# Kernel tuning notes

Measured on AMD Instinct MI355X. Metric: run time of the kernel, lower is better.

Reference implementation:

```python
import jax, jax.numpy as jnp
import numpy as np

NEG = -1e30  # finite stand-in for -inf so softmax grads stay clean


def setup_inputs() -> dict:
    key = jax.random.key(0)
    k1, k2 = jax.random.split(key)
    C, D = 8192, 512
    gt_class_embeddings = jax.random.normal(k1, (C, D), dtype=jnp.float32)
    w = jax.random.normal(k2, (C, D), dtype=jnp.float32)
    return {"gt_class_embeddings": gt_class_embeddings, "w": w}


def reference(gt_class_embeddings, w):
    # L2-normalize class embeddings, cosine-similarity matrix S (diag == 1)
    G = gt_class_embeddings / jnp.linalg.norm(gt_class_embeddings, axis=-1, keepdims=True)
    S = G @ G.T  # [C, C]
    C = S.shape[0]
    off_diag = ~jnp.eye(C, dtype=bool)

    # seSoftmax: per-row softmax over entries != 1 (off-diagonal); diagonal stays 1
    P = jax.nn.softmax(jnp.where(off_diag, S, NEG), axis=-1)
    S2 = jnp.where(off_diag, P, 1.0)

    # argsort(-S2)[1] == most similar (diag value 1 always ranks first),
    # argsort(-S2)[-1] == least similar == row min (softmax values < 1)
    ms = jnp.argmax(jnp.where(off_diag, S2, NEG), axis=-1)  # [C]
    ls = jnp.argmin(jnp.where(off_diag, S2, -NEG), axis=-1)  # [C]

    rows = jnp.arange(C)
    margin = S2[rows, ms] - S2[rows, ls]  # [C]

    d_ms = jnp.sqrt(jnp.sum((w - w[ms]) ** 2, axis=-1))  # [C]
    d_ls = jnp.sqrt(jnp.sum((w - w[ls]) ** 2, axis=-1))  # [C]

    loss = jnp.mean(jnp.maximum(0.0, d_ms - d_ls + margin))
    return loss
```

## Files before the change

### kernel.cpp

```cpp
#include <hip/hip_runtime.h>
#include <math.h>

#define CDIM 8192
#define DDIM 512
#define NEGF -3.0e38f
#define POSF  3.0e38f

#define BM 128
#define NSLOT (CDIM / BM)

typedef __attribute__((ext_vector_type(8))) short bf16x8;
typedef __attribute__((ext_vector_type(4))) float f32x4;

__device__ __forceinline__ unsigned short f2bf(float x) {
    unsigned int u = __float_as_uint(x);
    u += 0x7fffu + ((u >> 16) & 1u);
    return (unsigned short)(u >> 16);
}
__device__ __forceinline__ float bf2f(unsigned short h) {
    return __uint_as_float(((unsigned int)h) << 16);
}
__device__ __forceinline__ void gld16(const void* g, void* l) {
    __builtin_amdgcn_global_load_lds(
        (__attribute__((address_space(1))) void*)(void*)g,
        (__attribute__((address_space(3))) void*)l, 16, 0, 0);
}

__global__ __launch_bounds__(256) void k_prep(const float* __restrict__ g,
                                              unsigned short* __restrict__ hi,
                                              unsigned short* __restrict__ lo) {
    const int wave = threadIdx.x >> 6;
    const int lane = threadIdx.x & 63;
    const int row = blockIdx.x * 4 + wave;
    const float4* src = (const float4*)(g + (size_t)row * DDIM);
    const float4 a = src[lane * 2];
    const float4 b = src[lane * 2 + 1];
    float s = a.x * a.x + a.y * a.y + a.z * a.z + a.w * a.w +
              b.x * b.x + b.y * b.y + b.z * b.z + b.w * b.w;
#pragma unroll
    for (int m = 1; m < 64; m <<= 1) s += __shfl_xor(s, m, 64);
    const float rn = rsqrtf(s);
    const float y[8] = {a.x * rn, a.y * rn, a.z * rn, a.w * rn,
                        b.x * rn, b.y * rn, b.z * rn, b.w * rn};
    unsigned int hv[4], lv[4];
#pragma unroll
    for (int i = 0; i < 4; ++i) {
        const unsigned short h0 = f2bf(y[2 * i]);
        const unsigned short h1 = f2bf(y[2 * i + 1]);
        const unsigned short l0 = f2bf(y[2 * i] - bf2f(h0));
        const unsigned short l1 = f2bf(y[2 * i + 1] - bf2f(h1));
        hv[i] = (unsigned int)h0 | ((unsigned int)h1 << 16);
        lv[i] = (unsigned int)l0 | ((unsigned int)l1 << 16);
    }
    uint4* dh = (uint4*)(hi + (size_t)row * DDIM + lane * 8);
    uint4* dl = (uint4*)(lo + (size_t)row * DDIM + lane * 8);
    *dh = make_uint4(hv[0], hv[1], hv[2], hv[3]);
    *dl = make_uint4(lv[0], lv[1], lv[2], lv[3]);
}

__device__ __constant__ unsigned char OSUP[28] = {
    1, 2, 10,   3, 11, 19,   4, 12, 20,   28, 5, 13,
    21, 29, 37, 6,   14, 22, 30, 38,   46, 7, 15, 23,   31, 39, 47, 55};

__global__ __launch_bounds__(256, 3) void k_simstats(
    const unsigned short* __restrict__ ghi, const unsigned short* __restrict__ glo,
    float* __restrict__ pmax, float* __restrict__ pmin, float* __restrict__ pZ,
    int* __restrict__ pamax, int* __restrict__ pamin) {
    const int bid = blockIdx.x;
    const int xcd = bid & 7;
    const int off = bid >> 3;
    int I, J;
    if (xcd < 4) {
        if (off < 72) {
            const int s = xcd * 2 + (off >= 36);
            const int u = (off >= 36) ? off - 36 : off;
            int jj = 0;
            while ((jj + 1) * (jj + 2) / 2 <= u) ++jj;
            const int ii = u - jj * (jj + 1) / 2;
            I = s * 8 + ii; J = s * 8 + jj;
        } else {
            const int sup = (off - 72) >> 6;
            const int u = (off - 72) & 63;
            const int code = OSUP[xcd * 3 + sup];
            I = (code >> 3) * 8 + (u & 7);
            J = (code & 7) * 8 + (u >> 3);
        }
    } else {
        if (off >= 256) return;
        const int sup = off >> 6;
        const int u = off & 63;
        const int code = OSUP[12 + (xcd - 4) * 4 + sup];
        I = (code >> 3) * 8 + (u & 7);
        J = (code & 7) * 8 + (u >> 3);
    }

    __shared__ unsigned short SH[6 * 4096];
    const int t = threadIdx.x;
    const int wave = t >> 6;
    const int lane = t & 63;
    const int lanelo = lane & 15;
    const int quad = lane >> 4;
    const int wr = wave & 1;
    const int wc = wave >> 1;

    const int srow = t >> 2;
    const int scolb = ((t & 3) ^ ((t >> 3) & 3)) << 4;

    const int fsl = (quad ^ ((lanelo >> 1) & 3)) << 3;
    const int aoff = (wr * 64 + lanelo) * 32 + fsl;
    const int boff = (wc * 64 + lanelo) * 32 + fsl;

    float* rm  = (float*)SH;
    float* rz  = rm + 256;
    float* rmn = rz + 256;
    int*   ra  = (int*)(rmn + 256);
    int*   ran = ra + 256;
    float* cm  = (float*)(SH + 4096);
    float* cz  = cm + 256;
    float* cmn = cz + 256;
    int*   ca  = (int*)(cmn + 256);
    int*   can = ca + 256;

    const int i0 = I * BM;
    const int j0 = J * BM;
    const bool isdiag = (I == J);

    f32x4 acc[4][4];
#pragma unroll
    for (int rt = 0; rt < 4; ++rt)
#pragma unroll
        for (int ct = 0; ct < 4; ++ct)
            acc[rt][ct] = (f32x4){0.f, 0.f, 0.f, 0.f};

    const char* baseAh = (const char*)ghi + (size_t)(i0 + srow) * 1024 + scolb;
    const char* baseAl = (const char*)glo + (size_t)(i0 + srow) * 1024 + scolb;
    const char* baseBh = (const char*)ghi + (size_t)(j0 + srow) * 1024 + scolb;
    const char* baseBl = (const char*)glo + (size_t)(j0 + srow) * 1024 + scolb;

    auto STG = [&](const char* gbase, int ks, int s) {
        char* const d = (char*)SH + s * 8192 + t * 16;
        const size_t cb = (size_t)ks * 64;
        gld16(gbase + cb, d);
        gld16(gbase + 65536 + cb, d + 4096);
    };

    const int rAH[6] = {0, 4, 2, 1, 5, 3};
    const int rBL[6] = {1, 5, 3, 0, 4, 2};
    const int rBH[6] = {2, 1, 5, 3, 0, 4};
    const int rAL[6] = {3, 0, 4, 2, 1, 5};

    STG(baseAh, 0, 0);
    STG(baseBl, 0, 1);
    STG(baseBh, 0, 2);
    STG(baseAl, 0, 3);

    bf16x8 ah[4], bh[4];
#pragma unroll
    for (int ks = 0; ks < 16; ++ks) {
        const int m = ks % 6;
        const int m2 = (ks + 1) % 6;
        if (ks < 15) { STG(baseAh, ks + 1, rAH[m2]); STG(baseBl, ks + 1, rBL[m2]); }
        if (ks < 15) asm volatile("s_waitcnt vmcnt(8)" ::: "memory");
        else         asm volatile("s_waitcnt vmcnt(4)" ::: "memory");
        __builtin_amdgcn_s_barrier();
        asm volatile("" ::: "memory");
        {
            const unsigned short* pA = SH + rAH[m] * 4096;
            const unsigned short* pB = SH + rBL[m] * 4096;
            bf16x8 bl[4];
#pragma unroll
            for (int rt = 0; rt < 4; ++rt) ah[rt] = *(const bf16x8*)&pA[aoff + rt * 512];
#pragma unroll
            for (int ct = 0; ct < 4; ++ct) bl[ct] = *(const bf16x8*)&pB[boff + ct * 512];
            __builtin_amdgcn_s_setprio(1);
#pragma unroll
            for (int ct = 0; ct < 4; ++ct)
#pragma unroll
                for (int rt = 0; rt < 4; ++rt)
                    acc[rt][ct] = __builtin_amdgcn_mfma_f32_16x16x32_bf16(
                        ah[rt], bl[ct], acc[rt][ct], 0, 0, 0);
            __builtin_amdgcn_s_setprio(0);
        }
        asm volatile("s_waitcnt lgkmcnt(0)" ::: "memory");
        __builtin_amdgcn_s_barrier();
        asm volatile("" ::: "memory");
        if (ks < 15) STG(baseBh, ks + 1, rBH[m2]);
        if (ks < 15) asm volatile("s_waitcnt vmcnt(8)" ::: "memory");
        else         asm volatile("s_waitcnt vmcnt(2)" ::: "memory");
        __builtin_amdgcn_s_barrier();
        asm volatile("" ::: "memory");
        {
            const unsigned short* pB = SH + rBH[m] * 4096;
#pragma unroll
            for (int ct = 0; ct < 4; ++ct) bh[ct] = *(const bf16x8*)&pB[boff + ct * 512];
            __builtin_amdgcn_s_setprio(1);
#pragma unroll
            for (int ct = 0; ct < 4; ++ct)
#pragma unroll
                for (int rt = 0; rt < 4; ++rt)
                    acc[rt][ct] = __builtin_amdgcn_mfma_f32_16x16x32_bf16(
                        ah[rt], bh[ct], acc[rt][ct], 0, 0, 0);
            __builtin_amdgcn_s_setprio(0);
        }
        asm volatile("s_waitcnt lgkmcnt(0)" ::: "memory");
        __builtin_amdgcn_s_barrier();
        asm volatile("" ::: "memory");
        if (ks < 15) STG(baseAl, ks + 1, rAL[m2]);
        if (ks < 15) asm volatile("s_waitcnt vmcnt(8)" ::: "memory");
        else         asm volatile("s_waitcnt vmcnt(0)" ::: "memory");
        __builtin_amdgcn_s_barrier();
        asm volatile("" ::: "memory");
        {
            const unsigned short* pA = SH + rAL[m] * 4096;
            bf16x8 al[4];
#pragma unroll
            for (int rt = 0; rt < 4; ++rt) al[rt] = *(const bf16x8*)&pA[aoff + rt * 512];
            __builtin_amdgcn_s_setprio(1);
#pragma unroll
            for (int ct = 0; ct < 4; ++ct)
#pragma unroll
                for (int rt = 0; rt < 4; ++rt)
                    acc[rt][ct] = __builtin_amdgcn_mfma_f32_16x16x32_bf16(
                        al[rt], bh[ct], acc[rt][ct], 0, 0, 0);
            __builtin_amdgcn_s_setprio(0);
        }
        asm volatile("s_waitcnt lgkmcnt(0)" ::: "memory");
        __builtin_amdgcn_s_barrier();
        asm volatile("" ::: "memory");
    }

#pragma unroll
    for (int rt = 0; rt < 4; ++rt) {
#pragma unroll
        for (int r = 0; r < 4; ++r) {
            const int lrow = wr * 64 + rt * 16 + quad * 4 + r;
            float tmax = NEGF; int targ = 0;
            float tmin = POSF; int targn = 0;
            if (isdiag) {
                const int gi = i0 + lrow;
#pragma unroll
                for (int ct = 0; ct < 4; ++ct) {
                    const int gj = j0 + wc * 64 + ct * 16 + lanelo;
                    const float v = acc[rt][ct][r];
                    const bool dg = (gj == gi);
                    const float vM = dg ? NEGF : v;
                    const float vm = dg ? POSF : v;
                    if (vM > tmax) { tmax = vM; targ = gj; }
                    if (vm < tmin) { tmin = vm; targn = gj; }
                }
            } else {
#pragma unroll
                for (int ct = 0; ct < 4; ++ct) {
                    const int gj = j0 + wc * 64 + ct * 16 + lanelo;
                    const float v = acc[rt][ct][r];
                    if (v > tmax) { tmax = v; targ = gj; }
                    if (v < tmin) { tmin = v; targn = gj; }
                }
            }
#pragma unroll
            for (int msk = 1; msk < 16; msk <<= 1) {
                const float v2 = __shfl_xor(tmax, msk, 64);
                const int i2 = __shfl_xor(targ, msk, 64);
                if (v2 > tmax) { tmax = v2; targ = i2; }
                const float v3 = __shfl_xor(tmin, msk, 64);
                const int i3 = __shfl_xor(targn, msk, 64);
                if (v3 < tmin) { tmin = v3; targn = i3; }
            }
            if (lanelo == 0) {
                const int o = wc * 128 + lrow;
                rm[o] = tmax; rmn[o] = tmin;
                ra[o] = targ; ran[o] = targn;
            }
        }
    }

    if (!isdiag) {
#pragma unroll
        for (int ct = 0; ct < 4; ++ct) {
            const int lcol = wc * 64 + ct * 16 + lanelo;
            float tmax = NEGF; int targ = 0;
            float tmin = POSF; int targn = 0;
#pragma unroll
            for (int rt = 0; rt < 4; ++rt)
#pragma unroll
                for (int r = 0; r < 4; ++r) {
                    const int gi = i0 + wr * 64 + rt * 16 + quad * 4 + r;
                    const float v = acc[rt][ct][r];
                    if (v > tmax) { tmax = v; targ = gi; }
                    if (v < tmin) { tmin = v; targn = gi; }
                }
#pragma unroll
            for (int msk = 16; msk < 64; msk <<= 1) {
                const float m2v = __shfl_xor(tmax, msk, 64);
                const int i2 = __shfl_xor(targ, msk, 64);
                if (m2v > tmax) { tmax = m2v; targ = i2; }
                const float mn2 = __shfl_xor(tmin, msk, 64);
                const int in2 = __shfl_xor(targn, msk, 64);
                if (mn2 < tmin) { tmin = mn2; targn = in2; }
            }
            if (quad == 0) {
                const int o = wr * 128 + lcol;
                cm[o] = tmax; cmn[o] = tmin;
                ca[o] = targ; can[o] = targn;
            }
        }
    }

#pragma unroll
    for (int rt = 0; rt < 4; ++rt)
#pragma unroll
        for (int ct = 0; ct < 4; ++ct)
#pragma unroll
            for (int r = 0; r < 4; ++r)
                acc[rt][ct][r] = __expf(acc[rt][ct][r] - 1.f);
    if (isdiag && wr == wc) {
#pragma unroll
        for (int rt = 0; rt < 4; ++rt)
#pragma unroll
            for (int r = 0; r < 4; ++r)
                if (lanelo == quad * 4 + r) acc[rt][rt][r] = 0.f;
    }

#pragma unroll
    for (int rt = 0; rt < 4; ++rt)
#pragma unroll
        for (int r = 0; r < 4; ++r) {
            float s = acc[rt][0][r] + acc[rt][1][r] +
                      acc[rt][2][r] + acc[rt][3][r];
#pragma unroll
            for (int msk = 1; msk < 16; msk <<= 1) s += __shfl_xor(s, msk, 64);
            if (lanelo == 0)
                rz[wc * 128 + wr * 64 + rt * 16 + quad * 4 + r] = s;
        }

    if (!isdiag) {
#pragma unroll
        for (int ct = 0; ct < 4; ++ct) {
            float s = 0.f;
#pragma unroll
            for (int rt = 0; rt < 4; ++rt)
                s += acc[rt][ct][0] + acc[rt][ct][1] +
                     acc[rt][ct][2] + acc[rt][ct][3];
#pragma unroll
            for (int msk = 16; msk < 64; msk <<= 1) s += __shfl_xor(s, msk, 64);
            if (quad == 0)
                cz[wr * 128 + wc * 64 + ct * 16 + lanelo] = s;
        }
    }

    __syncthreads();

    if (t < BM) {
        const float m0 = rm[t], m1 = rm[128 + t];
        float vmax = m0; int imax = ra[t];
        if (m1 > vmax) { vmax = m1; imax = ra[128 + t]; }
        float vmin = rmn[t]; int imin = ran[t];
        if (rmn[128 + t] < vmin) { vmin = rmn[128 + t]; imin = ran[128 + t]; }
        const size_t o = (size_t)J * CDIM + i0 + t;
        pmax[o] = vmax; pmin[o] = vmin; pZ[o] = rz[t] + rz[128 + t];
        pamax[o] = imax; pamin[o] = imin;
    } else if (!isdiag) {
        const int tt = t - BM;
        const float m0 = cm[tt], m1 = cm[128 + tt];
        float vmax = m0; int imax = ca[tt];
        if (m1 > vmax) { vmax = m1; imax = ca[128 + tt]; }
        float vmin = cmn[tt]; int imin = can[tt];
        if (cmn[128 + tt] < vmin) { vmin = cmn[128 + tt]; imin = can[128 + tt]; }
        const size_t o = (size_t)I * CDIM + j0 + tt;
        pmax[o] = vmax; pmin[o] = vmin; pZ[o] = cz[tt] + cz[128 + tt];
        pamax[o] = imax; pamin[o] = imin;
    }
}

__global__ __launch_bounds__(256) void k_lossc(
    const float* __restrict__ pmax, const float* __restrict__ pmin,
    const float* __restrict__ pZ, const int* __restrict__ pamax,
    const int* __restrict__ pamin, const float* __restrict__ w,
    float* __restrict__ vals) {
    const int wave = threadIdx.x >> 6;
    const int lane = threadIdx.x & 63;
    const int row = blockIdx.x * 4 + wave;
    const size_t o = (size_t)lane * CDIM + row;
    float v = pmax[o]; int a = pamax[o];
    float u = pmin[o]; int b = pamin[o];
    float z = pZ[o];
#pragma unroll
    for (int msk = 1; msk < 64; msk <<= 1) {
        const float v2 = __shfl_xor(v, msk, 64);
        const int i2 = __shfl_xor(a, msk, 64);
        if (v2 > v) { v = v2; a = i2; }
        const float v3 = __shfl_xor(u, msk, 64);
        const int i3 = __shfl_xor(b, msk, 64);
        if (v3 < u) { u = v3; b = i3; }
        z += __shfl_xor(z, msk, 64);
    }
    const float margin = (1.f - __expf(u - v)) * __expf(v - 1.f) / z;
    const int jm = a, jl = b;

    const float4* wi = (const float4*)(w + (size_t)row * DDIM);
    const float4* wm = (const float4*)(w + (size_t)jm * DDIM);
    const float4* wl = (const float4*)(w + (size_t)jl * DDIM);
    float sm = 0.f, sl = 0.f;
#pragma unroll
    for (int h = 0; h < 2; ++h) {
        const int idx = h * 64 + lane;
        const float4 x = wi[idx];
        const float4 y = wm[idx];
        const float4 c = wl[idx];
        float d;
        d = x.x - y.x; sm = fmaf(d, d, sm);
        d = x.y - y.y; sm = fmaf(d, d, sm);
        d = x.z - y.z; sm = fmaf(d, d, sm);
        d = x.w - y.w; sm = fmaf(d, d, sm);
        d = x.x - c.x; sl = fmaf(d, d, sl);
        d = x.y - c.y; sl = fmaf(d, d, sl);
        d = x.z - c.z; sl = fmaf(d, d, sl);
        d = x.w - c.w; sl = fmaf(d, d, sl);
    }
#pragma unroll
    for (int msk = 1; msk < 64; msk <<= 1) {
        sm += __shfl_xor(sm, msk, 64);
        sl += __shfl_xor(sl, msk, 64);
    }
    if (lane == 0) {
        const float val = sqrtf(sm) - sqrtf(sl) + margin;
        vals[row] = val > 0.f ? val : 0.f;
    }
}

__global__ __launch_bounds__(256) void k_final(const float* __restrict__ vals,
                                               float* __restrict__ out) {
    __shared__ float red[256];
    float s = 0.f;
    for (int i = threadIdx.x; i < CDIM; i += 256) s += vals[i];
    red[threadIdx.x] = s;
    __syncthreads();
#pragma unroll
    for (int k = 128; k > 0; k >>= 1) {
        if (threadIdx.x < (unsigned)k) red[threadIdx.x] += red[threadIdx.x + k];
        __syncthreads();
    }
    if (threadIdx.x == 0) out[0] = red[0] * (1.0f / CDIM);
}

extern "C" void kernel_launch(void* const* d_in, const int* in_sizes, int n_in,
                              void* d_out, int out_size, void* d_ws, size_t ws_size,
                              hipStream_t stream) {
    const float* g = (const float*)d_in[0];
    const float* w = (const float*)d_in[1];
    float* out = (float*)d_out;

    unsigned short* ghi = (unsigned short*)d_ws;
    unsigned short* glo = ghi + (size_t)CDIM * DDIM;
    float* p = (float*)(glo + (size_t)CDIM * DDIM);
    float* pmax = p;      p += (size_t)NSLOT * CDIM;
    float* pmin = p;      p += (size_t)NSLOT * CDIM;
    float* pZ = p;        p += (size_t)NSLOT * CDIM;
    int* pamax = (int*)p; p += (size_t)NSLOT * CDIM;
    int* pamin = (int*)p; p += (size_t)NSLOT * CDIM;
    float* vals = p;      p += CDIM;

    k_prep<<<CDIM / 4, 256, 0, stream>>>(g, ghi, glo);
    k_simstats<<<2112, 256, 0, stream>>>(ghi, glo, pmax, pmin, pZ, pamax, pamin);
    k_lossc<<<CDIM / 4, 256, 0, stream>>>(pmax, pmin, pZ, pamax, pamin, w, vals);
    k_final<<<1, 256, 0, stream>>>(vals, out);
}
```

Before: 228.4 us.

## Use 256x128 tiles with 512-thread blocks and triple-buffered K pipeline

Enlarges the symmetric similarity tile from 128x128 to 256x128 per block with 8 waves, halving the block count and replacing the XCD-aware supertile schedule with a simple triangular enumeration over (I, J) pairs. The K loop moves from a six-slot per-operand rotation to a three-stage buffer holding the full A and B hi/lo tiles, prefetching two steps ahead. Diagonal handling is generalized to two partial-diagonal tile types. The aim is more operand reuse per loaded byte and fewer blocks, at the cost of much larger LDS use (144KB per block) and lower occupancy, and the simpler schedule drops the L2/XCD locality mapping.

```diff
diff --git a/kernel.cpp b/kernel.cpp
--- a/kernel.cpp
+++ b/kernel.cpp
@@ -6,8 +6,7 @@
 #define NEGF -3.0e38f
 #define POSF  3.0e38f
 
-#define BM 128
-#define NSLOT (CDIM / BM)
+#define NSLOT 64
 
 typedef __attribute__((ext_vector_type(8))) short bf16x8;
 typedef __attribute__((ext_vector_type(4))) float f32x4;
@@ -58,50 +57,30 @@
     *dl = make_uint4(lv[0], lv[1], lv[2], lv[3]);
 }
 
-__device__ __constant__ unsigned char OSUP[28] = {
-    1, 2, 10,   3, 11, 19,   4, 12, 20,   28, 5, 13,
-    21, 29, 37, 6,   14, 22, 30, 38,   46, 7, 15, 23,   31, 39, 47, 55};
-
-__global__ __launch_bounds__(256, 3) void k_simstats(
+__global__ __launch_bounds__(512, 2) void k_simstats(
     const unsigned short* __restrict__ ghi, const unsigned short* __restrict__ glo,
     float* __restrict__ pmax, float* __restrict__ pmin, float* __restrict__ pZ,
     int* __restrict__ pamax, int* __restrict__ pamin) {
     const int bid = blockIdx.x;
-    const int xcd = bid & 7;
-    const int off = bid >> 3;
-    int I, J;
-    if (xcd < 4) {
-        if (off < 72) {
-            const int s = xcd * 2 + (off >= 36);
-            const int u = (off >= 36) ? off - 36 : off;
-            int jj = 0;
-            while ((jj + 1) * (jj + 2) / 2 <= u) ++jj;
-            const int ii = u - jj * (jj + 1) / 2;
-            I = s * 8 + ii; J = s * 8 + jj;
-        } else {
-            const int sup = (off - 72) >> 6;
-            const int u = (off - 72) & 63;
-            const int code = OSUP[xcd * 3 + sup];
-            I = (code >> 3) * 8 + (u & 7);
-            J = (code & 7) * 8 + (u >> 3);
-        }
-    } else {
-        if (off >= 256) return;
-        const int sup = off >> 6;
-        const int u = off & 63;
-        const int code = OSUP[12 + (xcd - 4) * 4 + sup];
-        I = (code >> 3) * 8 + (u & 7);
-        J = (code & 7) * 8 + (u >> 3);
-    }
-
-    __shared__ unsigned short SH[6 * 4096];
+    const int e = (bid & 7) * 132 + (bid >> 3);
+    int J = 0, base = 0;
+    while (true) {
+        const int cnt = (J >> 1) + 1;
+        if (e < base + cnt) break;
+        base += cnt; ++J;
+    }
+    const int I = e - base;
+    const bool typeD0 = (J == 2 * I);
+    const bool typeD1 = (J == 2 * I + 1);
+
+    __shared__ unsigned short SH[3 * 24576];
     const int t = threadIdx.x;
     const int wave = t >> 6;
     const int lane = t & 63;
     const int lanelo = lane & 15;
     const int quad = lane >> 4;
-    const int wr = wave & 1;
-    const int wc = wave >> 1;
+    const int wr = wave >> 1;
+    const int wc = wave & 1;
 
     const int srow = t >> 2;
     const int scolb = ((t & 3) ^ ((t >> 3) & 3)) << 4;
@@ -111,19 +90,18 @@
     const int boff = (wc * 64 + lanelo) * 32 + fsl;
 
     float* rm  = (float*)SH;
-    float* rz  = rm + 256;
-    float* rmn = rz + 256;
-    int*   ra  = (int*)(rmn + 256);
-    int*   ran = ra + 256;
-    float* cm  = (float*)(SH + 4096);
-    float* cz  = cm + 256;
-    float* cmn = cz + 256;
-    int*   ca  = (int*)(cmn + 256);
-    int*   can = ca + 256;
-
-    const int i0 = I * BM;
-    const int j0 = J * BM;
-    const bool isdiag = (I == J);
+    float* rmn = rm + 512;
+    float* rz  = rmn + 512;
+    int*   ra  = (int*)(rz + 512);
+    int*   ran = ra + 512;
+    float* cm  = (float*)(ran + 512);
+    float* cmn = cm + 512;
+    float* cz  = cmn + 512;
+    int*   ca  = (int*)(cz + 512);
+    int*   can = ca + 512;
+
+    const int i0 = I * 256;
+    const int j0 = J * 128;
 
     f32x4 acc[4][4];
 #pragma unroll
@@ -137,41 +115,43 @@
     const char* baseBh = (const char*)ghi + (size_t)(j0 + srow) * 1024 + scolb;
     const char* baseBl = (const char*)glo + (size_t)(j0 + srow) * 1024 + scolb;
 
-    auto STG = [&](const char* gbase, int ks, int s) {
-        char* const d = (char*)SH + s * 8192 + t * 16;
+    auto STG_A = [&](int ks, int b, int half) {
+        char* d = (char*)SH + b * 49152 + half * 16384 + t * 16;
+        const char* gb = half ? baseAl : baseAh;
         const size_t cb = (size_t)ks * 64;
-        gld16(gbase + cb, d);
-        gld16(gbase + 65536 + cb, d + 4096);
+        gld16(gb + cb, d);
+        gld16(gb + 131072 + cb, d + 8192);
     };
-
-    const int rAH[6] = {0, 4, 2, 1, 5, 3};
-    const int rBL[6] = {1, 5, 3, 0, 4, 2};
-    const int rBH[6] = {2, 1, 5, 3, 0, 4};
-    const int rAL[6] = {3, 0, 4, 2, 1, 5};
-
-    STG(baseAh, 0, 0);
-    STG(baseBl, 0, 1);
-    STG(baseBh, 0, 2);
-    STG(baseAl, 0, 3);
-
-    bf16x8 ah[4], bh[4];
+    auto STG_B = [&](int ks, int b, int half) {
+        char* d = (char*)SH + b * 49152 + 32768 + half * 8192 + t * 16;
+        const char* gb = half ? baseBl : baseBh;
+        gld16(gb + (size_t)ks * 64, d);
+    };
+
+    STG_A(0, 0, 0); STG_A(0, 0, 1); STG_B(0, 0, 0); STG_B(0, 0, 1);
+    STG_A(1, 1, 0); STG_A(1, 1, 1); STG_B(1, 1, 0); STG_B(1, 1, 1);
+    asm volatile("s_waitcnt vmcnt(6)" ::: "memory");
+    __builtin_amdgcn_s_barrier();
+    asm volatile("" ::: "memory");
+
 #pragma unroll
     for (int ks = 0; ks < 16; ++ks) {
-        const int m = ks % 6;
-        const int m2 = (ks + 1) % 6;
-        if (ks < 15) { STG(baseAh, ks + 1, rAH[m2]); STG(baseBl, ks + 1, rBL[m2]); }
-        if (ks < 15) asm volatile("s_waitcnt vmcnt(8)" ::: "memory");
-        else         asm volatile("s_waitcnt vmcnt(4)" ::: "memory");
-        __builtin_amdgcn_s_barrier();
-        asm volatile("" ::: "memory");
+        const unsigned short* buf = SH + (ks % 3) * 24576;
+        const int sb = (ks + 2) % 3;
+        const bool st = (ks <= 13);
+        bf16x8 ah[4], bh[4];
         {
-            const unsigned short* pA = SH + rAH[m] * 4096;
-            const unsigned short* pB = SH + rBL[m] * 4096;
+            if (st) STG_A(ks + 2, sb, 0);
             bf16x8 bl[4];
 #pragma unroll
-            for (int rt = 0; rt < 4; ++rt) ah[rt] = *(const bf16x8*)&pA[aoff + rt * 512];
-#pragma unroll
-            for (int ct = 0; ct < 4; ++ct) bl[ct] = *(const bf16x8*)&pB[boff + ct * 512];
+            for (int rt = 0; rt < 4; ++rt)
+                ah[rt] = *(const bf16x8*)&buf[aoff + rt * 512];
+#pragma unroll
+            for (int ct = 0; ct < 4; ++ct)
+                bl[ct] = *(const bf16x8*)&buf[20480 + boff + ct * 512];
+            asm volatile("" ::: "memory");
+            __builtin_amdgcn_s_barrier();
+            asm volatile("s_waitcnt lgkmcnt(0)" ::: "memory");
             __builtin_amdgcn_s_setprio(1);
 #pragma unroll
             for (int ct = 0; ct < 4; ++ct)
@@ -180,19 +160,18 @@
                     acc[rt][ct] = __builtin_amdgcn_mfma_f32_16x16x32_bf16(
                         ah[rt], bl[ct], acc[rt][ct], 0, 0, 0);
             __builtin_amdgcn_s_setprio(0);
-        }
-        asm volatile("s_waitcnt lgkmcnt(0)" ::: "memory");
-        __builtin_amdgcn_s_barrier();
-        asm volatile("" ::: "memory");
-        if (ks < 15) STG(baseBh, ks + 1, rBH[m2]);
-        if (ks < 15) asm volatile("s_waitcnt vmcnt(8)" ::: "memory");
-        else         asm volatile("s_waitcnt vmcnt(2)" ::: "memory");
-        __builtin_amdgcn_s_barrier();
-        asm volatile("" ::: "memory");
+            asm volatile("" ::: "memory");
+            __builtin_amdgcn_s_barrier();
+            asm volatile("" ::: "memory");
+        }
         {
-            const unsigned short* pB = SH + rBH[m] * 4096;
-#pragma unroll
-            for (int ct = 0; ct < 4; ++ct) bh[ct] = *(const bf16x8*)&pB[boff + ct * 512];
+            if (st) STG_A(ks + 2, sb, 1);
+#pragma unroll
+            for (int ct = 0; ct < 4; ++ct)
+                bh[ct] = *(const bf16x8*)&buf[16384 + boff + ct * 512];
+            asm volatile("" ::: "memory");
+            __builtin_amdgcn_s_barrier();
+            asm volatile("s_waitcnt lgkmcnt(0)" ::: "memory");
             __builtin_amdgcn_s_setprio(1);
 #pragma unroll
             for (int ct = 0; ct < 4; ++ct)
@@ -201,20 +180,21 @@
                     acc[rt][ct] = __builtin_amdgcn_mfma_f32_16x16x32_bf16(
                         ah[rt], bh[ct], acc[rt][ct], 0, 0, 0);
             __builtin_amdgcn_s_setprio(0);
-        }
-        asm volatile("s_waitcnt lgkmcnt(0)" ::: "memory");
-        __builtin_amdgcn_s_barrier();
-        asm volatile("" ::: "memory");
-        if (ks < 15) STG(baseAl, ks + 1, rAL[m2]);
-        if (ks < 15) asm volatile("s_waitcnt vmcnt(8)" ::: "memory");
-        else         asm volatile("s_waitcnt vmcnt(0)" ::: "memory");
-        __builtin_amdgcn_s_barrier();
-        asm volatile("" ::: "memory");
+            asm volatile("" ::: "memory");
+            __builtin_amdgcn_s_barrier();
+            asm volatile("" ::: "memory");
+        }
         {
-            const unsigned short* pA = SH + rAL[m] * 4096;
+            if (st) { STG_B(ks + 2, sb, 0); STG_B(ks + 2, sb, 1); }
             bf16x8 al[4];
 #pragma unroll
-            for (int rt = 0; rt < 4; ++rt) al[rt] = *(const bf16x8*)&pA[aoff + rt * 512];
+            for (int rt = 0; rt < 4; ++rt)
+                al[rt] = *(const bf16x8*)&buf[8192 + aoff + rt * 512];
+            if (ks <= 13) asm volatile("s_waitcnt vmcnt(6)" ::: "memory");
+            else if (ks == 14) asm volatile("s_waitcnt vmcnt(0)" ::: "memory");
+            asm volatile("" ::: "memory");
+            __builtin_amdgcn_s_barrier();
+            asm volatile("s_waitcnt lgkmcnt(0)" ::: "memory");
             __builtin_amdgcn_s_setprio(1);
 #pragma unroll
             for (int ct = 0; ct < 4; ++ct)
@@ -223,39 +203,31 @@
                     acc[rt][ct] = __builtin_amdgcn_mfma_f32_16x16x32_bf16(
                         al[rt], bh[ct], acc[rt][ct], 0, 0, 0);
             __builtin_amdgcn_s_setprio(0);
-        }
-        asm volatile("s_waitcnt lgkmcnt(0)" ::: "memory");
-        __builtin_amdgcn_s_barrier();
-        asm volatile("" ::: "memory");
-    }
+            asm volatile("" ::: "memory");
+            __builtin_amdgcn_s_barrier();
+            asm volatile("" ::: "memory");
+        }
+    }
+
+    const bool mask_d = (typeD0 && wr < 2) || (typeD1 && wr >= 2);
 
 #pragma unroll
     for (int rt = 0; rt < 4; ++rt) {
 #pragma unroll
         for (int r = 0; r < 4; ++r) {
             const int lrow = wr * 64 + rt * 16 + quad * 4 + r;
+            const int gi = i0 + lrow;
             float tmax = NEGF; int targ = 0;
             float tmin = POSF; int targn = 0;
-            if (isdiag) {
-                const int gi = i0 + lrow;
-#pragma unroll
-                for (int ct = 0; ct < 4; ++ct) {
-                    const int gj = j0 + wc * 64 + ct * 16 + lanelo;
-                    const float v = acc[rt][ct][r];
-                    const bool dg = (gj == gi);
-                    const float vM = dg ? NEGF : v;
-                    const float vm = dg ? POSF : v;
-                    if (vM > tmax) { tmax = vM; targ = gj; }
-                    if (vm < tmin) { tmin = vm; targn = gj; }
-                }
-            } else {
-#pragma unroll
-                for (int ct = 0; ct < 4; ++ct) {
-                    const int gj = j0 + wc * 64 + ct * 16 + lanelo;
-                    const float v = acc[rt][ct][r];
-                    if (v > tmax) { tmax = v; targ = gj; }
-                    if (v < tmin) { tmin = v; targn = gj; }
-                }
+#pragma unroll
+            for (int ct = 0; ct < 4; ++ct) {
+                const int gj = j0 + wc * 64 + ct * 16 + lanelo;
+                const float v = acc[rt][ct][r];
+                const bool dg = mask_d && (gj == gi);
+                const float vM = dg ? NEGF : v;
+                const float vm = dg ? POSF : v;
+                if (vM > tmax) { tmax = vM; targ = gj; }
+                if (vm < tmin) { tmin = vm; targn = gj; }
             }
 #pragma unroll
             for (int msk = 1; msk < 16; msk <<= 1) {
@@ -267,14 +239,15 @@
                 if (v3 < tmin) { tmin = v3; targn = i3; }
             }
             if (lanelo == 0) {
-                const int o = wc * 128 + lrow;
+                const int o = wc * 256 + lrow;
                 rm[o] = tmax; rmn[o] = tmin;
                 ra[o] = targ; ran[o] = targn;
             }
         }
     }
 
-    if (!isdiag) {
+    const bool col_ok = (!typeD0 && !typeD1) || (typeD1 && wr < 2);
+    if (col_ok) {
 #pragma unroll
         for (int ct = 0; ct < 4; ++ct) {
             const int lcol = wc * 64 + ct * 16 + lanelo;
@@ -313,7 +286,8 @@
 #pragma unroll
             for (int r = 0; r < 4; ++r)
                 acc[rt][ct][r] = __expf(acc[rt][ct][r] - 1.f);
-    if (isdiag && wr == wc) {
+    if ((typeD0 && wr < 2 && wr == wc) ||
+        (typeD1 && wr >= 2 && (wr - 2) == wc)) {
 #pragma unroll
         for (int rt = 0; rt < 4; ++rt)
 #pragma unroll
@@ -330,10 +304,10 @@
 #pragma unroll
             for (int msk = 1; msk < 16; msk <<= 1) s += __shfl_xor(s, msk, 64);
             if (lanelo == 0)
-                rz[wc * 128 + wr * 64 + rt * 16 + quad * 4 + r] = s;
-        }
-
-    if (!isdiag) {
+                rz[wc * 256 + wr * 64 + rt * 16 + quad * 4 + r] = s;
+        }
+
+    if (col_ok) {
 #pragma unroll
         for (int ct = 0; ct < 4; ++ct) {
             float s = 0.f;
@@ -350,25 +324,33 @@
 
     __syncthreads();
 
-    if (t < BM) {
-        const float m0 = rm[t], m1 = rm[128 + t];
-        float vmax = m0; int imax = ra[t];
-        if (m1 > vmax) { vmax = m1; imax = ra[128 + t]; }
-        float vmin = rmn[t]; int imin = ran[t];
-        if (rmn[128 + t] < vmin) { vmin = rmn[128 + t]; imin = ran[128 + t]; }
-        const size_t o = (size_t)J * CDIM + i0 + t;
-        pmax[o] = vmax; pmin[o] = vmin; pZ[o] = rz[t] + rz[128 + t];
-        pamax[o] = imax; pamin[o] = imin;
-    } else if (!isdiag) {
-        const int tt = t - BM;
-        const float m0 = cm[tt], m1 = cm[128 + tt];
-        float vmax = m0; int imax = ca[tt];
-        if (m1 > vmax) { vmax = m1; imax = ca[128 + tt]; }
-        float vmin = cmn[tt]; int imin = can[tt];
-        if (cmn[128 + tt] < vmin) { vmin = cmn[128 + tt]; imin = can[128 + tt]; }
-        const size_t o = (size_t)I * CDIM + j0 + tt;
-        pmax[o] = vmax; pmin[o] = vmin; pZ[o] = cz[tt] + cz[128 + tt];
-        pamax[o] = imax; pamin[o] = imin;
+    if (t < 256) {
+        if (!(typeD0 && t >= 128)) {
+            const float m0 = rm[t], m1 = rm[256 + t];
+            float vmax = m0; int imax = ra[t];
+            if (m1 > vmax) { vmax = m1; imax = ra[256 + t]; }
+            float vmin = rmn[t]; int imin = ran[t];
+            if (rmn[256 + t] < vmin) { vmin = rmn[256 + t]; imin = ran[256 + t]; }
+            const size_t o = (size_t)J * CDIM + i0 + t;
+            pmax[o] = vmax; pmin[o] = vmin; pZ[o] = rz[t] + rz[256 + t];
+            pamax[o] = imax; pamin[o] = imin;
+        }
+    } else {
+        const int tt = t - 256;
+        const int h = tt >> 7;
+        const int col = tt & 127;
+        const bool ok = (!typeD0 && !typeD1) || (typeD1 && h == 0);
+        if (ok) {
+            const int b0 = h * 256 + col, b1 = h * 256 + 128 + col;
+            const float m0 = cm[b0], m1 = cm[b1];
+            float vmax = m0; int imax = ca[b0];
+            if (m1 > vmax) { vmax = m1; imax = ca[b1]; }
+            float vmin = cmn[b0]; int imin = can[b0];
+            if (cmn[b1] < vmin) { vmin = cmn[b1]; imin = can[b1]; }
+            const size_t o = (size_t)(2 * I + h) * CDIM + j0 + col;
+            pmax[o] = vmax; pmin[o] = vmin; pZ[o] = cz[b0] + cz[b1];
+            pamax[o] = imax; pamin[o] = imin;
+        }
     }
 }
 
@@ -461,7 +443,7 @@
     float* vals = p;      p += CDIM;
 
     k_prep<<<CDIM / 4, 256, 0, stream>>>(g, ghi, glo);
-    k_simstats<<<2112, 256, 0, stream>>>(ghi, glo, pmax, pmin, pZ, pamax, pamin);
+    k_simstats<<<1056, 512, 0, stream>>>(ghi, glo, pmax, pmin, pZ, pamax, pamin);
     k_lossc<<<CDIM / 4, 256, 0, stream>>>(pmax, pmin, pZ, pamax, pamin, w, vals);
     k_final<<<1, 256, 0, stream>>>(vals, out);
 }
```

Result: slower. 270.6 us (+18.5%).
